# Optimization experiments

Measured on AMD Instinct MI355X. Metric: run time of the kernel, lower is better.

## Reference

```python
import jax, jax.numpy as jnp
import numpy as np

B = 2_097_152  # batch (even, pairs are (0,1),(2,3),...)
C = 25         # hardcoded: M = eye(25), logits have 25 classes
LAMDA = 0.01


def setup_inputs() -> dict:
    key = jax.random.key(0)
    k1, k2 = jax.random.split(key, 2)
    inputs = jax.random.normal(k1, (B, C), dtype=jnp.float32)
    labels = jax.random.randint(k2, (B,), 0, C)
    M = jnp.eye(C, dtype=jnp.float32)  # learned Mahalanobis matrix (init = identity, as in torch)
    return {"inputs": inputs, "labels": labels, "M": M}


def _loss(inputs, M, labels):
    # ---- metric_learning: pairs (2i, 2i+1) ----
    a, b = inputs[0::2], inputs[1::2]          # [P, C]
    la, lb = labels[0::2], labels[1::2]        # [P]
    d = jnp.abs(a - b)                         # [P, C]
    # ||M.T * d[:,None]||_F = sqrt(sum_i d[i]^2 * sum_j M[j,i]^2)
    colsq = jnp.sum(M * M, axis=0)             # [C]
    norms = jnp.sqrt((d * d) @ colsq)          # [P]

    same = la == lb                            # positive pair mask
    pos = jnp.where(same, norms, jnp.zeros_like(norms))
    distance_p = jnp.sum(pos)
    # Faithful to source bug: distance_n is OVERWRITTEN (not accumulated) on each
    # negative pair as distance_p_so_far + norm; final value comes from the LAST
    # negative pair (0 if none exist).
    excl_cum_p = jnp.cumsum(pos) - pos         # distance_p before each pair
    neg_vals = excl_cum_p + norms              # candidate distance_n per pair
    P = norms.shape[0]
    last_neg = jnp.max(jnp.where(~same, jnp.arange(P), -1))
    distance_n = jnp.where(last_neg >= 0,
                           jnp.take(neg_vals, jnp.maximum(last_neg, 0)),
                           jnp.float32(0.0))
    metric_loss = jax.nn.relu(1.0 + distance_p - distance_n)

    # ---- cross entropy (mean over batch) ----
    logp = jax.nn.log_softmax(inputs, axis=-1)                       # [B, C]
    ce = -jnp.mean(jnp.take_along_axis(logp, labels[:, None], axis=-1))

    return ce + LAMDA * metric_loss / 2.0


def reference(inputs, labels, M):
    return _loss(inputs, M, labels)
```

## Files before the change

### kernel.cpp

```cpp
#include <hip/hip_runtime.h>
#include <math.h>

namespace {

constexpr int C      = 25;
constexpr int ROWS   = 256;
constexpr int TILE_F = ROWS * C;
constexpr int NBLK   = 768;

typedef const __attribute__((address_space(1))) void* gp_t;
typedef __attribute__((address_space(3))) void* lp_t;

__device__ __forceinline__ void load16_lds(const float* g, float* l) {
  __builtin_amdgcn_global_load_lds((gp_t)g, (lp_t)l, 16, 0, 0);
}

__global__ __launch_bounds__(256)
void k_ce(const float* __restrict__ x, const int* __restrict__ labels, int B,
          double* __restrict__ ce_part, int* __restrict__ ln_part) {
  __shared__ float tile[2][TILE_F];
  __shared__ float wsum[4];
  __shared__ int   wmax[4];

  const int t      = threadIdx.x;
  const int ntiles = B / ROWS;

  float ce_local = 0.f;
  int   best     = -1;
  int   cur      = 0;

  const int ti0 = blockIdx.x;
  if (ti0 < ntiles) {
    const float* g = x + (size_t)ti0 * TILE_F;
#pragma unroll
    for (int k = 0; k < 6; ++k)
      load16_lds(g + (k * 256 + t) * 4, &tile[0][(k * 256 + t) * 4]);
    if (t < 64) load16_lds(g + (1536 + t) * 4, &tile[0][(1536 + t) * 4]);
  }

  for (int ti = ti0; ti < ntiles; ti += NBLK) {
    __syncthreads();

    const int tnext = ti + NBLK;
    if (tnext < ntiles) {
      const float* g = x + (size_t)tnext * TILE_F;
      float* buf = tile[cur ^ 1];
#pragma unroll
      for (int k = 0; k < 6; ++k)
        load16_lds(g + (k * 256 + t) * 4, &buf[(k * 256 + t) * 4]);
      if (t < 64) load16_lds(g + (1536 + t) * 4, &buf[(1536 + t) * 4]);
    }

    const float* r = &tile[cur][t * C];
    float e[C];
#pragma unroll
    for (int c = 0; c < C; ++c) e[c] = r[c];

    const int row = ti * ROWS + t;
    const int lab = labels[row];

    float m = e[0];
#pragma unroll
    for (int c = 1; c < C; ++c) m = fmaxf(m, e[c]);
    float s = 0.f, xl = 0.f;
#pragma unroll
    for (int c = 0; c < C; ++c) {
      s += __expf(e[c] - m);
      xl = (c == lab) ? e[c] : xl;
    }
    ce_local += (m + __logf(s)) - xl;

    const int nxt = __shfl_down(lab, 1, 64);
    if (((t & 1) == 0) && lab != nxt) best = row >> 1;

    cur ^= 1;
  }

#pragma unroll
  for (int off = 32; off; off >>= 1) {
    ce_local += __shfl_down(ce_local, off, 64);
    best = max(best, __shfl_down(best, off, 64));
  }
  const int lane = t & 63, wid = t >> 6;
  if (lane == 0) { wsum[wid] = ce_local; wmax[wid] = best; }
  __syncthreads();
  if (t == 0) {
    ce_part[blockIdx.x] = (double)((wsum[0] + wsum[1]) + (wsum[2] + wsum[3]));
    ln_part[blockIdx.x] = max(max(wmax[0], wmax[1]), max(wmax[2], wmax[3]));
  }
}

__global__ __launch_bounds__(256)
void k_fin(const float* __restrict__ x, const float* __restrict__ M,
           const double* __restrict__ ce_part, const int* __restrict__ ln_part,
           int P, int B, float* __restrict__ out) {
  __shared__ float  colsq[C];
  __shared__ double sred[4];
  __shared__ int    ired[4];
  __shared__ double tred[4];
  __shared__ int    s_last;

  const int t = threadIdx.x, lane = t & 63, wid = t >> 6;

  if (t < C) {
    float s = 0.f;
    for (int r = 0; r < C; ++r) {
      float m = M[r * C + t];
      s += m * m;
    }
    colsq[t] = s;
  }

  double ce = 0.0;
  int ln = -1;
  for (int i = t; i < NBLK; i += 256) {
    ce += ce_part[i];
    ln = max(ln, ln_part[i]);
  }
#pragma unroll
  for (int off = 32; off; off >>= 1) {
    ce += __shfl_down(ce, off, 64);
    ln = max(ln, __shfl_down(ln, off, 64));
  }
  if (lane == 0) { sred[wid] = ce; ired[wid] = ln; }
  __syncthreads();
  if (t == 0) s_last = max(max(ired[0], ired[1]), max(ired[2], ired[3]));
  __syncthreads();
  const int last_neg = s_last;

  double tail = 0.0;
  for (int p = last_neg + 1 + t; p < P; p += 256) {
    const float* e = x + (size_t)p * (2 * C);
    float s = 0.f;
#pragma unroll
    for (int c = 0; c < C; ++c) {
      float d = e[c] - e[C + c];
      s = fmaf(d * d, colsq[c], s);
    }
    tail += (double)sqrtf(s);
  }
  float norm_last = 0.f;
  if (t == 0 && last_neg >= 0) {
    const float* e = x + (size_t)last_neg * (2 * C);
    float s = 0.f;
#pragma unroll
    for (int c = 0; c < C; ++c) {
      float d = e[c] - e[C + c];
      s = fmaf(d * d, colsq[c], s);
    }
    norm_last = sqrtf(s);
  }
#pragma unroll
  for (int off = 32; off; off >>= 1) tail += __shfl_down(tail, off, 64);
  if (lane == 0) tred[wid] = tail;
  __syncthreads();
  if (t == 0) {
    double tl    = (tred[0] + tred[1]) + (tred[2] + tred[3]);
    double cesum = (sred[0] + sred[1]) + (sred[2] + sred[3]);
    double cem   = cesum / (double)B;
    float  ml    = fmaxf(1.0f + (float)tl - norm_last, 0.0f);
    out[0] = (float)(cem + 0.005 * (double)ml);
  }
}

}

extern "C" void kernel_launch(void* const* d_in, const int* in_sizes, int n_in,
                              void* d_out, int out_size, void* d_ws,
                              size_t ws_size, hipStream_t stream) {
  const float* x      = (const float*)d_in[0];
  const int*   labels = (const int*)d_in[1];
  const float* M      = (const float*)d_in[2];
  float*       out    = (float*)d_out;

  double* ce_part = (double*)d_ws;
  int*    ln_part = (int*)((char*)d_ws + NBLK * sizeof(double));

  const int B = in_sizes[1];
  const int P = B / 2;

  k_ce<<<NBLK, 256, 0, stream>>>(x, labels, B, ce_part, ln_part);
  k_fin<<<1, 256, 0, stream>>>(x, M, ce_part, ln_part, P, B, out);
}
```

Baseline: 44.48 us.

## Fuse CE and finalize kernels via cooperative grid sync, prefetch labels

```diff
diff --git a/kernel.cpp b/kernel.cpp
--- a/kernel.cpp
+++ b/kernel.cpp
@@ -1,12 +1,15 @@
 #include <hip/hip_runtime.h>
+#include <hip/hip_cooperative_groups.h>
 #include <math.h>
+
+namespace cg = cooperative_groups;
 
 namespace {
 
 constexpr int C      = 25;
 constexpr int ROWS   = 256;
 constexpr int TILE_F = ROWS * C;
-constexpr int NBLK   = 768;
+constexpr int NBLK   = 512;
 
 typedef const __attribute__((address_space(1))) void* gp_t;
 typedef __attribute__((address_space(3))) void* lp_t;
@@ -16,32 +19,42 @@
 }
 
 __global__ __launch_bounds__(256)
-void k_ce(const float* __restrict__ x, const int* __restrict__ labels, int B,
-          double* __restrict__ ce_part, int* __restrict__ ln_part) {
+void k_all(const float* __restrict__ x, const int* __restrict__ labels,
+           const float* __restrict__ M, int B,
+           double* __restrict__ ce_part, int* __restrict__ ln_part,
+           float* __restrict__ out) {
   __shared__ float tile[2][TILE_F];
   __shared__ float wsum[4];
   __shared__ int   wmax[4];
+  __shared__ float  colsq[C];
+  __shared__ double sred[4];
+  __shared__ int    ired[4];
+  __shared__ double tred[4];
+  __shared__ int    s_last;
 
   const int t      = threadIdx.x;
   const int ntiles = B / ROWS;
+  const int bid    = blockIdx.x;
 
   float ce_local = 0.f;
   int   best     = -1;
   int   cur      = 0;
 
-  const int ti0 = blockIdx.x;
-  if (ti0 < ntiles) {
-    const float* g = x + (size_t)ti0 * TILE_F;
+  int lab = 0;
+  if (bid < ntiles) {
+    const float* g = x + (size_t)bid * TILE_F;
 #pragma unroll
     for (int k = 0; k < 6; ++k)
       load16_lds(g + (k * 256 + t) * 4, &tile[0][(k * 256 + t) * 4]);
     if (t < 64) load16_lds(g + (1536 + t) * 4, &tile[0][(1536 + t) * 4]);
+    lab = labels[(size_t)bid * ROWS + t];
   }
 
-  for (int ti = ti0; ti < ntiles; ti += NBLK) {
+  for (int ti = bid; ti < ntiles; ti += NBLK) {
     __syncthreads();
 
     const int tnext = ti + NBLK;
+    int labn = 0;
     if (tnext < ntiles) {
       const float* g = x + (size_t)tnext * TILE_F;
       float* buf = tile[cur ^ 1];
@@ -49,15 +62,13 @@
       for (int k = 0; k < 6; ++k)
         load16_lds(g + (k * 256 + t) * 4, &buf[(k * 256 + t) * 4]);
       if (t < 64) load16_lds(g + (1536 + t) * 4, &buf[(1536 + t) * 4]);
+      labn = labels[(size_t)tnext * ROWS + t];
     }
 
     const float* r = &tile[cur][t * C];
     float e[C];
 #pragma unroll
     for (int c = 0; c < C; ++c) e[c] = r[c];
-
-    const int row = ti * ROWS + t;
-    const int lab = labels[row];
 
     float m = e[0];
 #pragma unroll
@@ -71,8 +82,9 @@
     ce_local += (m + __logf(s)) - xl;
 
     const int nxt = __shfl_down(lab, 1, 64);
-    if (((t & 1) == 0) && lab != nxt) best = row >> 1;
+    if (((t & 1) == 0) && lab != nxt) best = (ti * ROWS + t) >> 1;
 
+    lab = labn;
     cur ^= 1;
   }
 
@@ -85,28 +97,19 @@
   if (lane == 0) { wsum[wid] = ce_local; wmax[wid] = best; }
   __syncthreads();
   if (t == 0) {
-    ce_part[blockIdx.x] = (double)((wsum[0] + wsum[1]) + (wsum[2] + wsum[3]));
-    ln_part[blockIdx.x] = max(max(wmax[0], wmax[1]), max(wmax[2], wmax[3]));
+    ce_part[bid] = (double)((wsum[0] + wsum[1]) + (wsum[2] + wsum[3]));
+    ln_part[bid] = max(max(wmax[0], wmax[1]), max(wmax[2], wmax[3]));
   }
-}
+  __threadfence();
+  cg::this_grid().sync();
 
-__global__ __launch_bounds__(256)
-void k_fin(const float* __restrict__ x, const float* __restrict__ M,
-           const double* __restrict__ ce_part, const int* __restrict__ ln_part,
-           int P, int B, float* __restrict__ out) {
-  __shared__ float  colsq[C];
-  __shared__ double sred[4];
-  __shared__ int    ired[4];
-  __shared__ double tred[4];
-  __shared__ int    s_last;
-
-  const int t = threadIdx.x, lane = t & 63, wid = t >> 6;
+  if (bid != 0) return;
 
   if (t < C) {
     float s = 0.f;
-    for (int r = 0; r < C; ++r) {
-      float m = M[r * C + t];
-      s += m * m;
+    for (int r2 = 0; r2 < C; ++r2) {
+      float mm = M[r2 * C + t];
+      s += mm * mm;
     }
     colsq[t] = s;
   }
@@ -127,25 +130,26 @@
   if (t == 0) s_last = max(max(ired[0], ired[1]), max(ired[2], ired[3]));
   __syncthreads();
   const int last_neg = s_last;
+  const int P = B / 2;
 
   double tail = 0.0;
   for (int p = last_neg + 1 + t; p < P; p += 256) {
-    const float* e = x + (size_t)p * (2 * C);
+    const float* e2 = x + (size_t)p * (2 * C);
     float s = 0.f;
 #pragma unroll
     for (int c = 0; c < C; ++c) {
-      float d = e[c] - e[C + c];
+      float d = e2[c] - e2[C + c];
       s = fmaf(d * d, colsq[c], s);
     }
     tail += (double)sqrtf(s);
   }
   float norm_last = 0.f;
   if (t == 0 && last_neg >= 0) {
-    const float* e = x + (size_t)last_neg * (2 * C);
+    const float* e2 = x + (size_t)last_neg * (2 * C);
     float s = 0.f;
 #pragma unroll
     for (int c = 0; c < C; ++c) {
-      float d = e[c] - e[C + c];
+      float d = e2[c] - e2[C + c];
       s = fmaf(d * d, colsq[c], s);
     }
     norm_last = sqrtf(s);
@@ -176,9 +180,10 @@
   double* ce_part = (double*)d_ws;
   int*    ln_part = (int*)((char*)d_ws + NBLK * sizeof(double));
 
-  const int B = in_sizes[1];
-  const int P = B / 2;
+  int B = in_sizes[1];
 
-  k_ce<<<NBLK, 256, 0, stream>>>(x, labels, B, ce_part, ln_part);
-  k_fin<<<1, 256, 0, stream>>>(x, M, ce_part, ln_part, P, B, out);
+  void* args[] = {(void*)&x, (void*)&labels, (void*)&M, (void*)&B,
+                  (void*)&ce_part, (void*)&ln_part, (void*)&out};
+  hipLaunchCooperativeKernel((const void*)k_all, dim3(NBLK), dim3(256), args,
+                             0, stream);
 }
```

Result: slower. 145.5 us (+227.1%).
